# Performance work log

Measured on AMD Instinct MI355X. Metric: run time of the kernel, lower is better.

The kernel has to match this reference:

```python
import jax, jax.numpy as jnp
import numpy as np

N_NODES = 10000
N_EDGES = 160000
F_IN = 256
HEADS = 4
F_OUT = 256
NEG_SLOPE = 0.2  # PyG GATConv default negative_slope
EPS = 1e-5       # GraphNorm eps


def gat_conv(x, src, dst, W, a_src, a_dst, bias, concat):
    """PyG-style GATConv. x:[N,Fin], W:[Fin,H*C], a_src/a_dst:[H,C], bias:[H*C] or [C].
    src/dst already include self-loops (add_self_loops=True default)."""
    N = x.shape[0]
    H, C = a_src.shape
    h = (x @ W).reshape(N, H, C)                      # per-head projected features
    al_s = jnp.einsum('nhc,hc->nh', h, a_src)          # [N,H]
    al_d = jnp.einsum('nhc,hc->nh', h, a_dst)          # [N,H]
    e = jax.nn.leaky_relu(al_s[src] + al_d[dst], NEG_SLOPE)  # [E,H] raw scores
    # segment softmax over edges grouped by destination node
    m = jax.ops.segment_max(e, dst, num_segments=N)    # [N,H]; every node has a self-loop
    ex = jnp.exp(e - m[dst])
    denom = jax.ops.segment_sum(ex, dst, num_segments=N)
    alpha = ex / denom[dst]                            # [E,H]
    out = jax.ops.segment_sum(h[src] * alpha[:, :, None], dst, num_segments=N)  # [N,H,C]
    out = out.reshape(N, H * C) if concat else out.mean(axis=1)
    return out + bias


def graph_norm(x, w, b, ms):
    """PyG GraphNorm over a single graph: y = w*(x-ms*mean)/sqrt(var+eps)+b."""
    mean = x.mean(axis=0, keepdims=True)
    sh = x - ms * mean
    var = (sh * sh).mean(axis=0, keepdims=True)
    return w * sh / jnp.sqrt(var + EPS) + b


def setup_inputs() -> dict:
    key = jax.random.key(0)
    ks = jax.random.split(key, 12)
    H1 = HEADS * F_IN  # 1024
    s = 0.05
    return {
        'x': jax.random.normal(ks[0], (N_NODES, F_IN), jnp.float32),
        'edge_index': jax.random.randint(ks[1], (2, N_EDGES), 0, N_NODES, jnp.int64),
        'W1': jax.random.normal(ks[2], (F_IN, HEADS * F_IN), jnp.float32) * s,
        'att_src1': jax.random.normal(ks[3], (HEADS, F_IN), jnp.float32) * s,
        'att_dst1': jax.random.normal(ks[4], (HEADS, F_IN), jnp.float32) * s,
        'b1': jnp.zeros((H1,), jnp.float32),
        'gn_w': jnp.ones((H1,), jnp.float32),
        'gn_b': jnp.zeros((H1,), jnp.float32),
        'gn_ms': jnp.ones((H1,), jnp.float32),
        'W2': jax.random.normal(ks[5], (H1, F_OUT), jnp.float32) * s,
        'att_src2': jax.random.normal(ks[6], (1, F_OUT), jnp.float32) * s,
        'att_dst2': jax.random.normal(ks[7], (1, F_OUT), jnp.float32) * s,
        'b2': jnp.zeros((F_OUT,), jnp.float32),
    }


def reference(x, edge_index, W1, att_src1, att_dst1, b1, gn_w, gn_b, gn_ms,
              W2, att_src2, att_dst2, b2):
    N = x.shape[0]
    loop = jnp.arange(N, dtype=edge_index.dtype)
    src = jnp.concatenate([edge_index[0], loop])  # add_self_loops=True
    dst = jnp.concatenate([edge_index[1], loop])
    h = gat_conv(x, src, dst, W1, att_src1, att_dst1, b1, concat=True)   # [N, H*Fin]
    h = graph_norm(h, gn_w, gn_b, gn_ms)
    h = jax.nn.relu(h)
    # F.dropout(training=self.training): eval mode -> identity
    out = gat_conv(h, src, dst, W2, att_src2, att_dst2, b2, concat=False)  # [N, Fout]
    return out
```

## Files before the change

### kernel.cpp

```cpp
#include <hip/hip_runtime.h>
#include <hip/hip_bf16.h>

#define NNODES 10000
#define FIN    256
#define HEADS  4
#define H1DIM  1024
#define FOUT   256
#define NEG    0.2f
#define GNEPS  1e-5f
#define SLOTS  96

typedef unsigned short u16;
typedef __attribute__((ext_vector_type(8))) short bf16x8;
typedef __attribute__((ext_vector_type(4))) float f32x4;

__device__ __forceinline__ float bf2f(u16 u) {
    union { unsigned int i; float f; } v; v.i = ((unsigned int)u) << 16; return v.f;
}
__device__ __forceinline__ u16 f2bf(float f) {
    __hip_bfloat16 h = __float2bfloat16(f);
    union { __hip_bfloat16 h; u16 u; } v; v.h = h; return v.u;
}
__device__ __forceinline__ float lrelu(float v) { return v > 0.f ? v : NEG * v; }

__device__ __forceinline__ void gll16(const u16* g, u16* l) {
    __builtin_amdgcn_global_load_lds(
        (const __attribute__((address_space(1))) unsigned int*)g,
        (__attribute__((address_space(3))) unsigned int*)l, 16, 0, 0);
}

__device__ __forceinline__ void compute_flags(const int* ei, const u16* x,
                                              int& is64, int& isbf)
{
    int or_odd = ei[1] | ei[3] | ei[5] | ei[7] | ei[9] | ei[11];
    is64 = (or_odd == 0) ? 1 : 0;
    int sane = 1;
    for (int i = 0; i < 32; i += 2) {
        u16 w = x[i];
        int e = (w >> 7) & 0xFF;
        if (!(w == 0 || w == 0x8000 || (e >= 100 && e <= 150))) sane = 0;
    }
    isbf = sane;
}

struct CvtDesc { const void* src; float* dst; int n; };
struct CvtTable { CvtDesc d[9]; };

__global__ void pvec_kernel(const void* __restrict__ x, const int* __restrict__ ei,
                            const void* __restrict__ W1,
                            const void* __restrict__ as1, const void* __restrict__ ad1,
                            float* __restrict__ Pm,
                            int* __restrict__ flag, int* __restrict__ fflag)
{
    __shared__ int sfl[2];
    if (threadIdx.x == 0) {
        int is64, isbf;
        compute_flags(ei, (const u16*)x, is64, isbf);
        sfl[0] = is64; sfl[1] = isbf;
        if (blockIdx.x == 0) { flag[0] = is64; fflag[0] = isbf; }
    }
    __syncthreads();
    const int isbf = sfl[1];
    int wave = threadIdx.x >> 6, lane = threadIdx.x & 63;
    int idx = blockIdx.x * 4 + wave;
    int j = idx >> 8, k = idx & 255;
    int hd = j & 3;
    const void* av = (j < 4) ? as1 : ad1;
    int c = lane * 4;
    int widx = k * H1DIM + hd * FIN + c;
    int aidx = hd * FIN + c;
    float wv0, wv1, wv2, wv3, a0, a1, a2, a3;
    if (isbf) {
        ushort4 wu = *reinterpret_cast<const ushort4*>((const u16*)W1 + widx);
        ushort4 au = *reinterpret_cast<const ushort4*>((const u16*)av + aidx);
        wv0 = bf2f(wu.x); wv1 = bf2f(wu.y); wv2 = bf2f(wu.z); wv3 = bf2f(wu.w);
        a0 = bf2f(au.x); a1 = bf2f(au.y); a2 = bf2f(au.z); a3 = bf2f(au.w);
    } else {
        float4 wf = *reinterpret_cast<const float4*>((const float*)W1 + widx);
        float4 af = *reinterpret_cast<const float4*>((const float*)av + aidx);
        wv0 = wf.x; wv1 = wf.y; wv2 = wf.z; wv3 = wf.w;
        a0 = af.x; a1 = af.y; a2 = af.z; a3 = af.w;
    }
    float acc = wv0 * a0 + wv1 * a1 + wv2 * a2 + wv3 * a3;
#pragma unroll
    for (int off = 32; off > 0; off >>= 1)
        acc += __shfl_xor(acc, off, 64);
    if (lane == 0) Pm[j * FIN + k] = acc;
}

#define T0_N 2500
#define T1_N 256
#define T2_N 256
#define T3_N 9
#define T4_N 665
#define PREP_BLOCKS (T0_N + T1_N + T2_N + T3_N + T4_N)

__global__ void prep_kernel(const void* __restrict__ x, const int* __restrict__ ei,
                            const void* __restrict__ W1, const void* __restrict__ W2,
                            CvtTable smalls,
                            u16* __restrict__ xb, u16* __restrict__ W1t,
                            u16* __restrict__ W2t, const float* __restrict__ Pm,
                            int* __restrict__ cursor, int* __restrict__ ssort,
                            float* __restrict__ als, float* __restrict__ ald,
                            int NE, int Etot)
{
    __shared__ int sfl[2];
    __shared__ u16 tile[32][33];
    if (threadIdx.x == 0) {
        int is64, isbf;
        compute_flags(ei, (const u16*)x, is64, isbf);
        sfl[0] = is64; sfl[1] = isbf;
    }
    __syncthreads();
    const int is64 = sfl[0], isbf = sfl[1];
    const int b = blockIdx.x;
    const int tid = threadIdx.x;

    if (b < T0_N) {
        int i4 = (b * 256 + tid) * 4;
        ushort4 o;
        if (isbf) {
            o = *reinterpret_cast<const ushort4*>((const u16*)x + i4);
        } else {
            float4 v = *reinterpret_cast<const float4*>((const float*)x + i4);
            o.x = f2bf(v.x); o.y = f2bf(v.y); o.z = f2bf(v.z); o.w = f2bf(v.w);
        }
        *reinterpret_cast<ushort4*>(xb + i4) = o;
        int wave = tid >> 6, lane = tid & 63;
        int n = b * 4 + wave;
        float x0 = bf2f(o.x), x1 = bf2f(o.y), x2 = bf2f(o.z), x3 = bf2f(o.w);
        float r[8];
#pragma unroll
        for (int j = 0; j < 8; j++) {
            float4 p = *reinterpret_cast<const float4*>(Pm + j * FIN + lane * 4);
            r[j] = x0 * p.x + x1 * p.y + x2 * p.z + x3 * p.w;
        }
#pragma unroll
        for (int off = 32; off > 0; off >>= 1)
#pragma unroll
            for (int j = 0; j < 8; j++)
                r[j] += __shfl_xor(r[j], off, 64);
        if (lane == 0) {
            *reinterpret_cast<float4*>(als + n * 4) = make_float4(r[0], r[1], r[2], r[3]);
            *reinterpret_cast<float4*>(ald + n * 4) = make_float4(r[4], r[5], r[6], r[7]);
        }
    } else if (b < T0_N + T1_N + T2_N) {
        const int task1 = (b < T0_N + T1_N);
        const int bb = task1 ? (b - T0_N) : (b - T0_N - T1_N);
        const void* W = task1 ? W1 : W2;
        u16* Wt = task1 ? W1t : W2t;
        const int K = task1 ? FIN : H1DIM;
        const int N = task1 ? H1DIM : FOUT;
        int ntiles_n = N >> 5;
        int tk = bb / ntiles_n, tn = bb - tk * ntiles_n;
        if (tk >= (K >> 5)) return;
        int k0 = tk << 5, n0 = tn << 5;
        int r = tid >> 5, cdx = tid & 31;
#pragma unroll
        for (int i = 0; i < 4; i++) {
            int kk = i * 8 + r;
            int srcIdx = (k0 + kk) * N + n0 + cdx;
            u16 v = isbf ? ((const u16*)W)[srcIdx] : f2bf(((const float*)W)[srcIdx]);
            tile[kk][cdx] = v;
        }
        __syncthreads();
#pragma unroll
        for (int i = 0; i < 4; i++) {
            int nn = i * 8 + r;
            Wt[(size_t)(n0 + nn) * K + k0 + cdx] = tile[cdx][nn];
        }
    } else if (b < T0_N + T1_N + T2_N + T3_N) {
        const int bb = b - (T0_N + T1_N + T2_N);
        CvtDesc d = smalls.d[bb];
        int i4 = tid * 4;
        if (i4 >= d.n) return;
        if (isbf) {
            ushort4 u = *reinterpret_cast<const ushort4*>((const u16*)d.src + i4);
            *reinterpret_cast<float4*>(d.dst + i4) =
                make_float4(bf2f(u.x), bf2f(u.y), bf2f(u.z), bf2f(u.w));
        } else {
            *reinterpret_cast<float4*>(d.dst + i4) =
                *reinterpret_cast<const float4*>((const float*)d.src + i4);
        }
    } else {
        const int bb = b - (T0_N + T1_N + T2_N + T3_N);
        int e = bb * 256 + tid;
        if (e >= Etot) return;
        int src, dst;
        if (e < NE) {
            src = is64 ? ei[2 * e] : ei[e];
            dst = is64 ? ei[2 * (NE + e)] : ei[NE + e];
        } else {
            src = dst = e - NE;
        }
        if ((unsigned)dst >= NNODES) return;
        if ((unsigned)src >= NNODES) src = 0;
        int idx = atomicAdd(&cursor[dst], 1);
        if (idx < SLOTS) ssort[dst * SLOTS + idx] = src;
    }
}

__global__ void agg_x_kernel(const int* __restrict__ cursor, const int* __restrict__ ssort,
                             const float* __restrict__ als, const float* __restrict__ ald,
                             const u16* __restrict__ xb, u16* __restrict__ zbuf)
{
    const int wave = threadIdx.x >> 6, lane = threadIdx.x & 63;
    const int n = blockIdx.x * 4 + wave;
    const bool active = (n < NNODES);
    int e0 = 0, e1 = 0;
    float4 adv = make_float4(0.f, 0.f, 0.f, 0.f);
    if (active) {
        e0 = n * SLOTS;
        e1 = e0 + min(cursor[n], SLOTS);
        adv = *reinterpret_cast<const float4*>(ald + n * 4);
    }

    float m0 = -1e30f, m1 = -1e30f, m2 = -1e30f, m3 = -1e30f;
    for (int e = e0 + lane; e < e1; e += 64) {
        int s = ssort[e];
        float4 av = *reinterpret_cast<const float4*>(als + s * 4);
        m0 = fmaxf(m0, lrelu(av.x + adv.x));
        m1 = fmaxf(m1, lrelu(av.y + adv.y));
        m2 = fmaxf(m2, lrelu(av.z + adv.z));
        m3 = fmaxf(m3, lrelu(av.w + adv.w));
    }
#pragma unroll
    for (int off = 32; off > 0; off >>= 1) {
        m0 = fmaxf(m0, __shfl_xor(m0, off, 64));
        m1 = fmaxf(m1, __shfl_xor(m1, off, 64));
        m2 = fmaxf(m2, __shfl_xor(m2, off, 64));
        m3 = fmaxf(m3, __shfl_xor(m3, off, 64));
    }

    __shared__ float wlds[4][128][4];
    __shared__ int schk[4];
    int myCh = active ? ((e1 - e0 + 127) >> 7) : 0;
    if (lane == 0) schk[wave] = myCh;
    __syncthreads();
    int mc = max(max(schk[0], schk[1]), max(schk[2], schk[3]));

    float d0 = 0, d1 = 0, d2 = 0, d3 = 0;
    float a[4][4];
#pragma unroll
    for (int h = 0; h < 4; h++)
#pragma unroll
        for (int c = 0; c < 4; c++) a[h][c] = 0.f;

    for (int ch = 0; ch < mc; ch++) {
        int cs = e0 + ch * 128;
        int ce = min(cs + 128, e1);
        if (ch < myCh) {
            for (int e = cs + lane; e < ce; e += 64) {
                int s = ssort[e];
                float4 av = *reinterpret_cast<const float4*>(als + s * 4);
                float w0 = __expf(lrelu(av.x + adv.x) - m0);
                float w1 = __expf(lrelu(av.y + adv.y) - m1);
                float w2 = __expf(lrelu(av.z + adv.z) - m2);
                float w3 = __expf(lrelu(av.w + adv.w) - m3);
                *reinterpret_cast<float4*>(&wlds[wave][e - cs][0]) = make_float4(w0, w1, w2, w3);
                d0 += w0; d1 += w1; d2 += w2; d3 += w3;
            }
        }
        __syncthreads();
        if (ch < myCh) {
#pragma unroll
            for (int half = 0; half < 2; half++) {
                int base = cs + half * 64;
                int cnt = ce - base;
                if (cnt <= 0) break;
                if (cnt > 64) cnt = 64;
                int sreg = (lane < cnt) ? ssort[base + lane] : 0;
                int wof = half * 64;
                int ee = 0;
                for (; ee + 3 < cnt; ee += 4) {
                    int s0 = __shfl(sreg, ee, 64);
                    int s1 = __shfl(sreg, ee + 1, 64);
                    int s2 = __shfl(sreg, ee + 2, 64);
                    int s3 = __shfl(sreg, ee + 3, 64);
                    ushort4 xv0 = *reinterpret_cast<const ushort4*>(xb + (size_t)s0 * FIN + lane * 4);
                    ushort4 xv1 = *reinterpret_cast<const ushort4*>(xb + (size_t)s1 * FIN + lane * 4);
                    ushort4 xv2 = *reinterpret_cast<const ushort4*>(xb + (size_t)s2 * FIN + lane * 4);
                    ushort4 xv3 = *reinterpret_cast<const ushort4*>(xb + (size_t)s3 * FIN + lane * 4);
                    float4 w0 = *reinterpret_cast<const float4*>(&wlds[wave][wof + ee][0]);
                    float4 w1 = *reinterpret_cast<const float4*>(&wlds[wave][wof + ee + 1][0]);
                    float4 w2 = *reinterpret_cast<const float4*>(&wlds[wave][wof + ee + 2][0]);
                    float4 w3 = *reinterpret_cast<const float4*>(&wlds[wave][wof + ee + 3][0]);
                    float p0, p1, p2, p3;
                    p0 = bf2f(xv0.x); p1 = bf2f(xv0.y); p2 = bf2f(xv0.z); p3 = bf2f(xv0.w);
                    a[0][0] += w0.x * p0; a[0][1] += w0.x * p1; a[0][2] += w0.x * p2; a[0][3] += w0.x * p3;
                    a[1][0] += w0.y * p0; a[1][1] += w0.y * p1; a[1][2] += w0.y * p2; a[1][3] += w0.y * p3;
                    a[2][0] += w0.z * p0; a[2][1] += w0.z * p1; a[2][2] += w0.z * p2; a[2][3] += w0.z * p3;
                    a[3][0] += w0.w * p0; a[3][1] += w0.w * p1; a[3][2] += w0.w * p2; a[3][3] += w0.w * p3;
                    p0 = bf2f(xv1.x); p1 = bf2f(xv1.y); p2 = bf2f(xv1.z); p3 = bf2f(xv1.w);
                    a[0][0] += w1.x * p0; a[0][1] += w1.x * p1; a[0][2] += w1.x * p2; a[0][3] += w1.x * p3;
                    a[1][0] += w1.y * p0; a[1][1] += w1.y * p1; a[1][2] += w1.y * p2; a[1][3] += w1.y * p3;
                    a[2][0] += w1.z * p0; a[2][1] += w1.z * p1; a[2][2] += w1.z * p2; a[2][3] += w1.z * p3;
                    a[3][0] += w1.w * p0; a[3][1] += w1.w * p1; a[3][2] += w1.w * p2; a[3][3] += w1.w * p3;
                    p0 = bf2f(xv2.x); p1 = bf2f(xv2.y); p2 = bf2f(xv2.z); p3 = bf2f(xv2.w);
                    a[0][0] += w2.x * p0; a[0][1] += w2.x * p1; a[0][2] += w2.x * p2; a[0][3] += w2.x * p3;
                    a[1][0] += w2.y * p0; a[1][1] += w2.y * p1; a[1][2] += w2.y * p2; a[1][3] += w2.y * p3;
                    a[2][0] += w2.z * p0; a[2][1] += w2.z * p1; a[2][2] += w2.z * p2; a[2][3] += w2.z * p3;
                    a[3][0] += w2.w * p0; a[3][1] += w2.w * p1; a[3][2] += w2.w * p2; a[3][3] += w2.w * p3;
                    p0 = bf2f(xv3.x); p1 = bf2f(xv3.y); p2 = bf2f(xv3.z); p3 = bf2f(xv3.w);
                    a[0][0] += w3.x * p0; a[0][1] += w3.x * p1; a[0][2] += w3.x * p2; a[0][3] += w3.x * p3;
                    a[1][0] += w3.y * p0; a[1][1] += w3.y * p1; a[1][2] += w3.y * p2; a[1][3] += w3.y * p3;
                    a[2][0] += w3.z * p0; a[2][1] += w3.z * p1; a[2][2] += w3.z * p2; a[2][3] += w3.z * p3;
                    a[3][0] += w3.w * p0; a[3][1] += w3.w * p1; a[3][2] += w3.w * p2; a[3][3] += w3.w * p3;
                }
                for (; ee < cnt; ee++) {
                    int s = __shfl(sreg, ee, 64);
                    ushort4 xv = *reinterpret_cast<const ushort4*>(xb + (size_t)s * FIN + lane * 4);
                    float4 w = *reinterpret_cast<const float4*>(&wlds[wave][wof + ee][0]);
                    float x0 = bf2f(xv.x), x1 = bf2f(xv.y), x2 = bf2f(xv.z), x3 = bf2f(xv.w);
                    a[0][0] += w.x * x0; a[0][1] += w.x * x1; a[0][2] += w.x * x2; a[0][3] += w.x * x3;
                    a[1][0] += w.y * x0; a[1][1] += w.y * x1; a[1][2] += w.y * x2; a[1][3] += w.y * x3;
                    a[2][0] += w.z * x0; a[2][1] += w.z * x1; a[2][2] += w.z * x2; a[2][3] += w.z * x3;
                    a[3][0] += w.w * x0; a[3][1] += w.w * x1; a[3][2] += w.w * x2; a[3][3] += w.w * x3;
                }
            }
        }
        __syncthreads();
    }
    if (!active) return;
#pragma unroll
    for (int off = 32; off > 0; off >>= 1) {
        d0 += __shfl_xor(d0, off, 64);
        d1 += __shfl_xor(d1, off, 64);
        d2 += __shfl_xor(d2, off, 64);
        d3 += __shfl_xor(d3, off, 64);
    }
    float invs[4];
    invs[0] = d0 > 0.f ? 1.f / d0 : 0.f;
    invs[1] = d1 > 0.f ? 1.f / d1 : 0.f;
    invs[2] = d2 > 0.f ? 1.f / d2 : 0.f;
    invs[3] = d3 > 0.f ? 1.f / d3 : 0.f;
#pragma unroll
    for (int h = 0; h < 4; h++) {
        ushort4 o;
        o.x = f2bf(a[h][0] * invs[h]);
        o.y = f2bf(a[h][1] * invs[h]);
        o.z = f2bf(a[h][2] * invs[h]);
        o.w = f2bf(a[h][3] * invs[h]);
        *reinterpret_cast<ushort4*>(zbuf + (size_t)h * NNODES * FIN + (size_t)n * FIN + lane * 4) = o;
    }
}

template<int BM, int BN, int MINW, bool NORM_A, bool BIAS, bool STATS, bool AL2>
__global__ void __launch_bounds__(256, MINW)
mfma_gemm(const u16* __restrict__ A, const u16* __restrict__ Bt,
          u16* __restrict__ C,
          const float* __restrict__ bias,
          float* __restrict__ gsum, float* __restrict__ gsum2,
          const float* __restrict__ gnw, const float* __restrict__ gnb,
          const float* __restrict__ gnms,
          const float* __restrict__ a2s, const float* __restrict__ a2d,
          float* __restrict__ al2s, float* __restrict__ al2d,
          int M, int K, int ldc, long aZ, long bZ, int cZ, int nbx)
{
    constexpr int MI = BM / 32;
    constexpr int NI = BN / 32;
    __shared__ u16 Alds[2][BM * 32];
    __shared__ u16 Blds[2][BN * 32];
    __shared__ float sc_lds[NORM_A ? H1DIM : 1];
    __shared__ float sh_lds[NORM_A ? H1DIM : 1];

    int bid = blockIdx.x;
    {
        int nwg = gridDim.x;
        int q = nwg >> 3, r = nwg & 7;
        int xcd = bid & 7, l = bid >> 3;
        bid = (xcd < r ? xcd * (q + 1) : r * (q + 1) + (xcd - r) * q) + l;
    }
    const int bx = bid % nbx;
    const int by = bid / nbx;

    const u16* Az = A + (long)blockIdx.z * aZ;
    const u16* Bz = Bt + (long)blockIdx.z * bZ;

    const int tid  = threadIdx.x;
    const int lane = tid & 63;
    const int wave = tid >> 6;
    const int wm = wave >> 1, wn = wave & 1;
    const int l15 = lane & 15, quad = lane >> 4;
    const int n0 = bx * BN;
    const int m0 = by * BM;

    if (NORM_A) {
        const float invN = 1.0f / (float)NNODES;
        for (int i = tid; i < K; i += 256) {
            float mean = gsum[i] * invN;
            float ex2  = gsum2[i] * invN;
            float msv  = gnms[i];
            float var  = ex2 - 2.f * msv * mean * mean + msv * msv * mean * mean;
            float sc   = gnw[i] * rsqrtf(fmaxf(var, 0.f) + GNEPS);
            sc_lds[i] = sc;
            sh_lds[i] = gnb[i] - sc * msv * mean;
        }
        __syncthreads();
    }

    const int lrw = lane >> 2, lcg = (lane & 3) * 8;
    auto stageB = [&](int c, int kt) {
#pragma unroll
        for (int s = wave; s < BN / 16; s += 4) {
            const u16* g = Bz + (size_t)(n0 + s * 16 + lrw) * K + kt + lcg;
            gll16(g, &Blds[c][s * 512]);
        }
    };
    auto stageAg = [&](int c, int kt) {
#pragma unroll
        for (int s = wave; s < BM / 16; s += 4) {
            const u16* g = Az + (size_t)(m0 + s * 16 + lrw) * K + kt + lcg;
            gll16(g, &Alds[c][s * 512]);
        }
    };
    const int arow = tid >> 2, acol = (tid & 3) * 8;
    uint4 apre;
    auto issueA = [&](int kt) {
        int gr = m0 + arow;
        apre = (gr < M)
            ? *reinterpret_cast<const uint4*>(Az + (size_t)gr * K + kt + acol)
            : make_uint4(0u, 0u, 0u, 0u);
    };
    auto commitA = [&](int c, int kt) {
        uint4 v = apre;
        int kr = kt + acol;
        float4 s0 = *reinterpret_cast<const float4*>(&sc_lds[kr]);
        float4 s1 = *reinterpret_cast<const float4*>(&sc_lds[kr + 4]);
        float4 h0 = *reinterpret_cast<const float4*>(&sh_lds[kr]);
        float4 h1 = *reinterpret_cast<const float4*>(&sh_lds[kr + 4]);
        float sc[8] = {s0.x, s0.y, s0.z, s0.w, s1.x, s1.y, s1.z, s1.w};
        float sh[8] = {h0.x, h0.y, h0.z, h0.w, h1.x, h1.y, h1.z, h1.w};
        u16* pv = reinterpret_cast<u16*>(&v);
#pragma unroll
        for (int j = 0; j < 8; j++)
            pv[j] = f2bf(fmaxf(0.f, bf2f(pv[j]) * sc[j] + sh[j]));
        *reinterpret_cast<uint4*>(&Alds[c][arow * 32 + acol]) = v;
    };

    f32x4 acc[MI][NI];
#pragma unroll
    for (int i = 0; i < MI; i++)
#pragma unroll
        for (int j = 0; j < NI; j++) acc[i][j] = (f32x4){0.f, 0.f, 0.f, 0.f};

    auto compute = [&](int c) {
        bf16x8 a_frag[MI], b_frag[NI];
#pragma unroll
        for (int mi = 0; mi < MI; mi++)
            a_frag[mi] = *reinterpret_cast<const bf16x8*>(
                &Alds[c][(wm * (BM / 2) + mi * 16 + l15) * 32 + quad * 8]);
#pragma unroll
        for (int ni = 0; ni < NI; ni++)
            b_frag[ni] = *reinterpret_cast<const bf16x8*>(
                &Blds[c][(wn * (BN / 2) + ni * 16 + l15) * 32 + quad * 8]);
#pragma unroll
        for (int mi = 0; mi < MI; mi++)
#pragma unroll
            for (int ni = 0; ni < NI; ni++)
                acc[mi][ni] = __builtin_amdgcn_mfma_f32_16x16x32_bf16(
                    a_frag[mi], b_frag[ni], acc[mi][ni], 0, 0, 0);
    };

    if (NORM_A) { issueA(0); commitA(0, 0); } else { stageAg(0, 0); }
    stageB(0, 0);
    __syncthreads();

    int cur = 0;
    for (int kt = 0; kt < K; kt += 32) {
        const bool nxt = (kt + 32 < K);
        if (nxt) {
            if (NORM_A) issueA(kt + 32); else stageAg(cur ^ 1, kt + 32);
            stageB(cur ^ 1, kt + 32);
        }
        compute(cur);
        if (nxt && NORM_A) commitA(cur ^ 1, kt + 32);
        __syncthreads();
        cur ^= 1;
    }

    float sacc[NI], qacc[NI];
#pragma unroll
    for (int ni = 0; ni < NI; ni++) { sacc[ni] = 0.f; qacc[ni] = 0.f; }

#pragma unroll
    for (int mi = 0; mi < MI; mi++) {
#pragma unroll
        for (int r = 0; r < 4; r++) {
            int row = m0 + wm * (BM / 2) + mi * 16 + quad * 4 + r;
            if (row >= M) continue;
            float ps = 0.f, pd = 0.f;
#pragma unroll
            for (int ni = 0; ni < NI; ni++) {
                int col = n0 + wn * (BN / 2) + ni * 16 + l15;
                float v = acc[mi][ni][r];
                if (BIAS) v += bias[blockIdx.z * cZ + col];
                if (STATS) { sacc[ni] += v; qacc[ni] += v * v; }
                if (AL2) { ps += v * a2s[col]; pd += v * a2d[col]; }
                C[(size_t)row * ldc + blockIdx.z * cZ + col] = f2bf(v);
            }
            if (AL2) {
                ps += __shfl_xor(ps, 1, 64); pd += __shfl_xor(pd, 1, 64);
                ps += __shfl_xor(ps, 2, 64); pd += __shfl_xor(pd, 2, 64);
                ps += __shfl_xor(ps, 4, 64); pd += __shfl_xor(pd, 4, 64);
                ps += __shfl_xor(ps, 8, 64); pd += __shfl_xor(pd, 8, 64);
                if (l15 == 0) {
                    atomicAdd(&al2s[row], ps);
                    atomicAdd(&al2d[row], pd);
                }
            }
        }
    }
    if (STATS) {
#pragma unroll
        for (int ni = 0; ni < NI; ni++) {
            float s = sacc[ni], q = qacc[ni];
            s += __shfl_xor(s, 16, 64); q += __shfl_xor(q, 16, 64);
            s += __shfl_xor(s, 32, 64); q += __shfl_xor(q, 32, 64);
            if (quad == 0) {
                int ch = blockIdx.z * cZ + n0 + wn * (BN / 2) + ni * 16 + l15;
                atomicAdd(&gsum[ch], s);
                atomicAdd(&gsum2[ch], q);
            }
        }
    }
}

__global__ void agg2_kernel(const int* __restrict__ cursor, const int* __restrict__ ssort,
                            const float* __restrict__ als, const float* __restrict__ ald,
                            const u16* __restrict__ h2, const float* __restrict__ b2,
                            const int* __restrict__ fflag, void* __restrict__ outv)
{
    const int wave = threadIdx.x >> 6, lane = threadIdx.x & 63;
    const int n = blockIdx.x * 4 + wave;
    const bool active = (n < NNODES);
    int e0 = 0, e1 = 0;
    float adv = 0.f;
    if (active) {
        e0 = n * SLOTS;
        e1 = e0 + min(cursor[n], SLOTS);
        adv = ald[n];
    }

    float m = -1e30f;
    for (int e = e0 + lane; e < e1; e += 64) {
        int s = ssort[e];
        m = fmaxf(m, lrelu(als[s] + adv));
    }
#pragma unroll
    for (int off = 32; off > 0; off >>= 1)
        m = fmaxf(m, __shfl_xor(m, off, 64));

    __shared__ float wlds[4][128];
    __shared__ int schk[4];
    int myCh = active ? ((e1 - e0 + 127) >> 7) : 0;
    if (lane == 0) schk[wave] = myCh;
    __syncthreads();
    int mc = max(max(schk[0], schk[1]), max(schk[2], schk[3]));

    float d = 0.f, a0 = 0.f, a1 = 0.f, a2 = 0.f, a3 = 0.f;
    for (int ch = 0; ch < mc; ch++) {
        int cs = e0 + ch * 128;
        int ce = min(cs + 128, e1);
        if (ch < myCh) {
            for (int e = cs + lane; e < ce; e += 64) {
                int s = ssort[e];
                float w = __expf(lrelu(als[s] + adv) - m);
                wlds[wave][e - cs] = w;
                d += w;
            }
        }
        __syncthreads();
        if (ch < myCh) {
#pragma unroll
            for (int half = 0; half < 2; half++) {
                int base = cs + half * 64;
                int cnt = ce - base;
                if (cnt <= 0) break;
                if (cnt > 64) cnt = 64;
                int sreg = (lane < cnt) ? ssort[base + lane] : 0;
                int wof = half * 64;
                int ee = 0;
                for (; ee + 3 < cnt; ee += 4) {
                    int s0 = __shfl(sreg, ee, 64);
                    int s1 = __shfl(sreg, ee + 1, 64);
                    int s2 = __shfl(sreg, ee + 2, 64);
                    int s3 = __shfl(sreg, ee + 3, 64);
                    ushort4 hv0 = *reinterpret_cast<const ushort4*>(h2 + (size_t)s0 * FOUT + lane * 4);
                    ushort4 hv1 = *reinterpret_cast<const ushort4*>(h2 + (size_t)s1 * FOUT + lane * 4);
                    ushort4 hv2 = *reinterpret_cast<const ushort4*>(h2 + (size_t)s2 * FOUT + lane * 4);
                    ushort4 hv3 = *reinterpret_cast<const ushort4*>(h2 + (size_t)s3 * FOUT + lane * 4);
                    float w0 = wlds[wave][wof + ee];
                    float w1 = wlds[wave][wof + ee + 1];
                    float w2 = wlds[wave][wof + ee + 2];
                    float w3 = wlds[wave][wof + ee + 3];
                    a0 += w0 * bf2f(hv0.x); a1 += w0 * bf2f(hv0.y);
                    a2 += w0 * bf2f(hv0.z); a3 += w0 * bf2f(hv0.w);
                    a0 += w1 * bf2f(hv1.x); a1 += w1 * bf2f(hv1.y);
                    a2 += w1 * bf2f(hv1.z); a3 += w1 * bf2f(hv1.w);
                    a0 += w2 * bf2f(hv2.x); a1 += w2 * bf2f(hv2.y);
                    a2 += w2 * bf2f(hv2.z); a3 += w2 * bf2f(hv2.w);
                    a0 += w3 * bf2f(hv3.x); a1 += w3 * bf2f(hv3.y);
                    a2 += w3 * bf2f(hv3.z); a3 += w3 * bf2f(hv3.w);
                }
                for (; ee < cnt; ee++) {
                    int s = __shfl(sreg, ee, 64);
                    float w = wlds[wave][wof + ee];
                    ushort4 hv = *reinterpret_cast<const ushort4*>(h2 + (size_t)s * FOUT + lane * 4);
                    a0 += w * bf2f(hv.x); a1 += w * bf2f(hv.y);
                    a2 += w * bf2f(hv.z); a3 += w * bf2f(hv.w);
                }
            }
        }
        __syncthreads();
    }
    if (!active) return;
#pragma unroll
    for (int off = 32; off > 0; off >>= 1)
        d += __shfl_xor(d, off, 64);
    float inv = d > 0.f ? 1.f / d : 0.f;
    int c = lane * 4;
    float4 bv = *reinterpret_cast<const float4*>(b2 + c);
    float r0 = a0 * inv + bv.x;
    float r1 = a1 * inv + bv.y;
    float r2 = a2 * inv + bv.z;
    float r3 = a3 * inv + bv.w;
    if (fflag[0]) {
        ushort4 o;
        o.x = f2bf(r0); o.y = f2bf(r1); o.z = f2bf(r2); o.w = f2bf(r3);
        *reinterpret_cast<ushort4*>((u16*)outv + (size_t)n * FOUT + c) = o;
    } else {
        *reinterpret_cast<float4*>((float*)outv + (size_t)n * FOUT + c) =
            make_float4(r0, r1, r2, r3);
    }
}

extern "C" void kernel_launch(void* const* d_in, const int* in_sizes, int n_in,
                              void* d_out, int out_size, void* d_ws, size_t ws_size,
                              hipStream_t stream)
{
    const void* x    = d_in[0];
    const int*  ei   = (const int*)d_in[1];
    const void* W1   = d_in[2];
    const void* as1  = d_in[3];
    const void* ad1  = d_in[4];
    const void* b1   = d_in[5];
    const void* gnw  = d_in[6];
    const void* gnb  = d_in[7];
    const void* gnms = d_in[8];
    const void* W2   = d_in[9];
    const void* as2  = d_in[10];
    const void* ad2  = d_in[11];
    const void* b2   = d_in[12];

    const int NE   = in_sizes[1] / 2;
    const int Etot = NE + NNODES;

    char* w = (char*)d_ws;
    size_t off = 0;
    auto carve = [&](size_t bytes) -> char* {
        char* p = w + off;
        off = (off + bytes + 255) & ~(size_t)255;
        return p;
    };
    int*   cursor = (int*)carve((size_t)NNODES * 4);
    float* gsum   = (float*)carve(1024 * 4);
    float* gsum2  = (float*)carve(1024 * 4);
    float* al2s   = (float*)carve((size_t)NNODES * 4);
    float* al2d   = (float*)carve((size_t)NNODES * 4);
    size_t zero_bytes = off;
    int*   flag   = (int*)carve(256);
    int*   fflag  = (int*)carve(256);
    int*   ssort  = (int*)carve((size_t)NNODES * SLOTS * 4);
    u16*   zbuf   = (u16*)carve((size_t)HEADS * NNODES * FIN * 2);
    u16*   out1b  = (u16*)carve((size_t)NNODES * H1DIM * 2);
    float* al1s   = (float*)carve((size_t)NNODES * HEADS * 4);
    float* al1d   = (float*)carve((size_t)NNODES * HEADS * 4);
    u16*   xb     = (u16*)carve((size_t)NNODES * FIN * 2);
    u16*   W1t    = (u16*)carve((size_t)H1DIM * FIN * 2);
    u16*   W2t    = (u16*)carve((size_t)FOUT * H1DIM * 2);
    float* Pm     = (float*)carve(8 * FIN * 4);
    float* b1f    = (float*)carve(1024 * 4);
    float* gnwf   = (float*)carve(1024 * 4);
    float* gnbf   = (float*)carve(1024 * 4);
    float* gnmsf  = (float*)carve(1024 * 4);
    float* as2f   = (float*)carve(256 * 4);
    float* ad2f   = (float*)carve(256 * 4);
    float* b2f    = (float*)carve(256 * 4);
    float* as1f   = (float*)carve(1024 * 4);
    float* ad1f   = (float*)carve(1024 * 4);
    (void)ws_size;

    u16* h2b = xb;

    hipMemsetAsync(d_ws, 0, zero_bytes, stream);

    pvec_kernel<<<512, 256, 0, stream>>>(x, ei, W1, as1, ad1, Pm, flag, fflag);

    {
        CvtTable tab;
        tab.d[0] = { b1,   b1f,   H1DIM };
        tab.d[1] = { gnw,  gnwf,  H1DIM };
        tab.d[2] = { gnb,  gnbf,  H1DIM };
        tab.d[3] = { gnms, gnmsf, H1DIM };
        tab.d[4] = { as2,  as2f,  FOUT };
        tab.d[5] = { ad2,  ad2f,  FOUT };
        tab.d[6] = { b2,   b2f,   FOUT };
        tab.d[7] = { as1,  as1f,  H1DIM };
        tab.d[8] = { ad1,  ad1f,  H1DIM };
        prep_kernel<<<PREP_BLOCKS, 256, 0, stream>>>(x, ei, W1, W2, tab,
                                                     xb, W1t, W2t, Pm, cursor, ssort,
                                                     al1s, al1d, NE, Etot);
    }
    agg_x_kernel<<<2500, 256, 0, stream>>>(cursor, ssort, al1s, al1d, xb, zbuf);
    {
        const int nbx = FIN / 128;
        const int nby = (NNODES + 63) / 64;
        dim3 grd(nbx * nby, 1, HEADS);
        mfma_gemm<64, 128, 4, false, true, true, false><<<grd, 256, 0, stream>>>(
            zbuf, W1t, out1b, b1f, gsum, gsum2, nullptr, nullptr, nullptr,
            nullptr, nullptr, nullptr, nullptr,
            NNODES, FIN, H1DIM, (long)NNODES * FIN, (long)FIN * FIN, FIN, nbx);
    }
    {
        const int nbx = FOUT / 64;
        const int nby = (NNODES + 63) / 64;
        dim3 grd(nbx * nby, 1, 1);
        mfma_gemm<64, 64, 4, true, false, false, true><<<grd, 256, 0, stream>>>(
            out1b, W2t, h2b, nullptr, gsum, gsum2, gnwf, gnbf, gnmsf,
            as2f, ad2f, al2s, al2d,
            NNODES, H1DIM, FOUT, 0L, 0L, 0, nbx);
    }
    agg2_kernel<<<2500, 256, 0, stream>>>(cursor, ssort, al2s, al2d, h2b, b2f, fflag, d_out);
}
```

Before: 199.6 us.

## Triple-buffer GEMM LDS staging with explicit vmcnt waits and raw barriers

```diff
diff --git a/kernel.cpp b/kernel.cpp
--- a/kernel.cpp
+++ b/kernel.cpp
@@ -28,6 +28,9 @@
         (const __attribute__((address_space(1))) unsigned int*)g,
         (__attribute__((address_space(3))) unsigned int*)l, 16, 0, 0);
 }
+
+#define ASM_VMCNT(N) asm volatile("s_waitcnt vmcnt(%0)" :: "i"(N) : "memory")
+#define ASM_LGKM0()  asm volatile("s_waitcnt lgkmcnt(0)" ::: "memory")
 
 __device__ __forceinline__ void compute_flags(const int* ei, const u16* x,
                                               int& is64, int& isbf)
@@ -359,8 +362,11 @@
 {
     constexpr int MI = BM / 32;
     constexpr int NI = BN / 32;
-    __shared__ u16 Alds[2][BM * 32];
-    __shared__ u16 Blds[2][BN * 32];
+    constexpr int GW = (NORM_A ? 0 : BM / 64) + BN / 64;
+    constexpr int VM_MAIN = 2 * GW + (NORM_A ? 1 : 0);
+    constexpr int VM_EPI  = GW + (NORM_A ? 1 : 0);
+    __shared__ u16 Alds[3][BM * 32];
+    __shared__ u16 Blds[3][BN * 32];
     __shared__ float sc_lds[NORM_A ? H1DIM : 1];
     __shared__ float sh_lds[NORM_A ? H1DIM : 1];
 
@@ -462,21 +468,39 @@
                     a_frag[mi], b_frag[ni], acc[mi][ni], 0, 0, 0);
     };
 
-    if (NORM_A) { issueA(0); commitA(0, 0); } else { stageAg(0, 0); }
+    const int nt = K / 32;
+
+    if (NORM_A) { issueA(0); } else { stageAg(0, 0); }
     stageB(0, 0);
+    if (!NORM_A) stageAg(1, 32);
+    stageB(1, 32);
+    if (NORM_A) commitA(0, 0);
     __syncthreads();
 
-    int cur = 0;
-    for (int kt = 0; kt < K; kt += 32) {
-        const bool nxt = (kt + 32 < K);
-        if (nxt) {
-            if (NORM_A) issueA(kt + 32); else stageAg(cur ^ 1, kt + 32);
-            stageB(cur ^ 1, kt + 32);
-        }
-        compute(cur);
-        if (nxt && NORM_A) commitA(cur ^ 1, kt + 32);
-        __syncthreads();
-        cur ^= 1;
+    for (int t = 0; t + 2 < nt; ++t) {
+        if (NORM_A) issueA((t + 1) * 32);
+        else        stageAg((t + 2) % 3, (t + 2) * 32);
+        stageB((t + 2) % 3, (t + 2) * 32);
+        ASM_VMCNT(VM_MAIN);
+        __builtin_amdgcn_s_barrier();
+        compute(t % 3);
+        if (NORM_A) commitA((t + 1) % 3, (t + 1) * 32);
+        ASM_LGKM0();
+        __builtin_amdgcn_s_barrier();
+    }
+    {
+        if (NORM_A) issueA((nt - 1) * 32);
+        ASM_VMCNT(VM_EPI);
+        __builtin_amdgcn_s_barrier();
+        compute((nt - 2) % 3);
+        if (NORM_A) commitA((nt - 1) % 3, (nt - 1) * 32);
+        ASM_LGKM0();
+        __builtin_amdgcn_s_barrier();
+    }
+    {
+        ASM_VMCNT(0);
+        __builtin_amdgcn_s_barrier();
+        compute((nt - 1) % 3);
     }
 
     float sacc[NI], qacc[NI];
```

New measurement: 201.8 us. About the same (+1.1%).
